# Performance work log

Hardware: AMD Instinct MI355X
Metric: run time of the kernel (lower is better)

The kernel has to match this reference:

```python
import jax, jax.numpy as jnp
import numpy as np

B = 16384      # batch
H = 1024       # latent_dim
C = 2          # output_dim (classes)
PPC = 24       # prototypes per class
P = C * PPC    # 48 total prototypes
EPS = 1e-4


def setup_inputs() -> dict:
    key = jax.random.key(0)
    k1, k2, k3, k4, k5 = jax.random.split(key, 5)
    specific_user = jax.random.normal(k1, (B, H), jnp.float32)
    shared_user = jax.random.normal(k2, (B, H), jnp.float32)
    prototype_vectors = jax.random.normal(k3, (P, H), jnp.float32)
    # last_layer weight set by set_last_layer_incorrect_connection(-0.5):
    # +1 for the prototype's own class, -0.5 elsewhere; shape [C, P]
    cls = np.arange(P) // PPC
    ident = (cls[None, :] == np.arange(C)[:, None]).astype(np.float32)
    last_layer_w = jnp.asarray(ident * 1.0 + (1.0 - ident) * (-0.5))
    # nn.Bilinear(H, H, 1): weight [1, H, H], bias [1]
    bilinear_w = jax.random.normal(k4, (1, H, H), jnp.float32) / np.sqrt(H)
    bilinear_b = jax.random.normal(k5, (1,), jnp.float32) * 0.01
    return {
        "specific_user": specific_user,
        "shared_user": shared_user,
        "prototype_vectors": prototype_vectors,
        "last_layer_w": last_layer_w,
        "bilinear_w": bilinear_w,
        "bilinear_b": bilinear_b,
        "flag": 1,
    }


def reference(specific_user, shared_user, prototype_vectors, last_layer_w,
              bilinear_w, bilinear_b, flag):
    # prototype_distances: squared euclid via mm + norms, then log-similarity
    x2 = jnp.sum(specific_user ** 2, axis=1, keepdims=True)          # [B,1]
    p2 = jnp.sum(prototype_vectors ** 2, axis=1)                     # [P]
    distance = -2.0 * (specific_user @ prototype_vectors.T) + x2 + p2[None, :]  # [B,P]
    similarity = jnp.log((distance + 1.0) / (distance + EPS))        # [B,P]
    logits = similarity @ last_layer_w.T                             # [B,C]

    # select the class's 24 prototypes (flag picks class 1 or 0; static int)
    idx = 1 if flag else 0
    sub = prototype_vectors.reshape(C, PPC, H)[idx]                  # [PPC,H]

    # prototype_subgraph_distances: per original broadcast, each row of
    # all_sim is the batch-mean of the log-similarity -> constant over batch.
    s2 = jnp.sum(sub ** 2, axis=1)                                   # [PPC]
    d = -2.0 * (specific_user @ sub.T) + x2 + s2[None, :]            # [B,PPC]
    sim = jnp.mean(jnp.log((d + 1.0) / (d + EPS)), axis=0)           # [PPC]
    jstar = jnp.argmax(sim)                                          # scalar
    chosen_proto = jnp.broadcast_to(sub[jstar], specific_user.shape) # [B,H]

    # nn.Bilinear(chosen_proto, shared_user) -> [B,1]
    pos = jnp.einsum('bi,ij,bj->b', chosen_proto, bilinear_w[0], shared_user)[:, None] + bilinear_b
    return (pos, shared_user, logits, distance)
```

## Files before the change

kernel.cpp:

```cpp
#include <hip/hip_runtime.h>
#include <hip/hip_bf16.h>

#define BATCH 16384
#define HD    1024
#define NP    48
#define PPC   24
#define EPSV  1e-4f

typedef __attribute__((ext_vector_type(8))) short  short8;
typedef __attribute__((ext_vector_type(4))) float  floatx4;

__device__ __forceinline__ float b2f(unsigned short s) {
    union { unsigned u; float f; } c; c.u = ((unsigned)s) << 16; return c.f;
}
__device__ __forceinline__ unsigned short f2bu(float f) {
    __hip_bfloat16 h = __float2bfloat16(f);
    union { __hip_bfloat16 h; unsigned short u; } c; c.h = h; return c.u;
}

__global__ __launch_bounds__(256) void k_prep(const float* __restrict__ proto,
                                              unsigned short* __restrict__ phi,
                                              unsigned short* __restrict__ plo,
                                              float* __restrict__ p2,
                                              float* __restrict__ vzero,
                                              float* __restrict__ gcol) {
    const int p = blockIdx.x;
    const int tid = threadIdx.x;
    if (p < 4)                        vzero[p * 256 + tid] = 0.f;
    else if (p == 4 && tid < NP)      gcol[tid] = 0.f;

    const float* row = proto + (size_t)p * HD;
    float acc = 0.f;
#pragma unroll
    for (int c = 0; c < 4; ++c) {
        const int k = c * 256 + tid;
        const float f = row[k];
        acc += f * f;
        const unsigned short h = f2bu(f);
        phi[(size_t)p * HD + k] = h;
        plo[(size_t)p * HD + k] = f2bu(f - b2f(h));
    }
#pragma unroll
    for (int m = 32; m >= 1; m >>= 1) acc += __shfl_xor(acc, m, 64);
    __shared__ float wsum[4];
    if ((tid & 63) == 0) wsum[tid >> 6] = acc;
    __syncthreads();
    if (tid == 0) p2[p] = wsum[0] + wsum[1] + wsum[2] + wsum[3];
}

__global__ __launch_bounds__(512, 8) void k_main(
    const float* __restrict__ x,
    const unsigned short* __restrict__ phi,
    const unsigned short* __restrict__ plo,
    const float* __restrict__ llw,
    const float* __restrict__ p2,
    float* __restrict__ gcol,
    float* __restrict__ out_logits,
    float* __restrict__ out_dist)
{
    __shared__ float lacc[8][64][13];
    __shared__ float lx2[8][16];
    const int wave = threadIdx.x >> 6;
    const int lane = threadIdx.x & 63;
    const int quad = lane >> 4;
    const int lr   = lane & 15;
    const int rb   = blockIdx.x * 16;
    const int ko   = wave * 128;

    const float* xr = x + (size_t)(rb + lr) * HD + ko + quad * 8;
    const unsigned short* ph0 = phi + (size_t)lr * HD + ko + quad * 8;
    const unsigned short* ph1 = ph0 + 16 * HD;
    const unsigned short* ph2 = ph0 + 32 * HD;
    const unsigned short* pl0 = plo + (size_t)lr * HD + ko + quad * 8;
    const unsigned short* pl1 = pl0 + 16 * HD;
    const unsigned short* pl2 = pl0 + 32 * HD;

    floatx4 acc0 = {0.f, 0.f, 0.f, 0.f};
    floatx4 acc1 = {0.f, 0.f, 0.f, 0.f};
    floatx4 acc2 = {0.f, 0.f, 0.f, 0.f};
    float x2p = 0.f;

#pragma unroll 2
    for (int kk = 0; kk < 4; ++kk) {
        const floatx4 xa = *(const floatx4*)(xr + kk * 32);
        const floatx4 xb = *(const floatx4*)(xr + kk * 32 + 4);
        short8 ah, al;
#pragma unroll
        for (int j = 0; j < 4; ++j) {
            const float f = xa[j];
            x2p += f * f;
            const unsigned short h = f2bu(f);
            ah[j] = (short)h;
            al[j] = (short)f2bu(f - b2f(h));
        }
#pragma unroll
        for (int j = 0; j < 4; ++j) {
            const float f = xb[j];
            x2p += f * f;
            const unsigned short h = f2bu(f);
            ah[4 + j] = (short)h;
            al[4 + j] = (short)f2bu(f - b2f(h));
        }
        const short8 bh0 = *(const short8*)(ph0 + kk * 32);
        const short8 bh1 = *(const short8*)(ph1 + kk * 32);
        const short8 bh2 = *(const short8*)(ph2 + kk * 32);
        const short8 bl0 = *(const short8*)(pl0 + kk * 32);
        const short8 bl1 = *(const short8*)(pl1 + kk * 32);
        const short8 bl2 = *(const short8*)(pl2 + kk * 32);
        acc0 = __builtin_amdgcn_mfma_f32_16x16x32_bf16(ah, bh0, acc0, 0, 0, 0);
        acc0 = __builtin_amdgcn_mfma_f32_16x16x32_bf16(ah, bl0, acc0, 0, 0, 0);
        acc0 = __builtin_amdgcn_mfma_f32_16x16x32_bf16(al, bh0, acc0, 0, 0, 0);
        acc1 = __builtin_amdgcn_mfma_f32_16x16x32_bf16(ah, bh1, acc1, 0, 0, 0);
        acc1 = __builtin_amdgcn_mfma_f32_16x16x32_bf16(ah, bl1, acc1, 0, 0, 0);
        acc1 = __builtin_amdgcn_mfma_f32_16x16x32_bf16(al, bh1, acc1, 0, 0, 0);
        acc2 = __builtin_amdgcn_mfma_f32_16x16x32_bf16(ah, bh2, acc2, 0, 0, 0);
        acc2 = __builtin_amdgcn_mfma_f32_16x16x32_bf16(ah, bl2, acc2, 0, 0, 0);
        acc2 = __builtin_amdgcn_mfma_f32_16x16x32_bf16(al, bh2, acc2, 0, 0, 0);
    }
    x2p += __shfl_xor(x2p, 16, 64);
    x2p += __shfl_xor(x2p, 32, 64);

#pragma unroll
    for (int r = 0; r < 4; ++r) {
        lacc[wave][lane][r]     = acc0[r];
        lacc[wave][lane][4 + r] = acc1[r];
        lacc[wave][lane][8 + r] = acc2[r];
    }
    if (quad == 0) lx2[wave][lr] = x2p;
    __syncthreads();
    if (wave != 0) return;

    float facc[12];
#pragma unroll
    for (int i = 0; i < 12; ++i) {
        float s = 0.f;
#pragma unroll
        for (int w = 0; w < 8; ++w) s += lacc[w][lane][i];
        facc[i] = s;
    }
    float x2full = 0.f;
#pragma unroll
    for (int w = 0; w < 8; ++w) x2full += lx2[w][lr];

    float s0[4] = {0.f, 0.f, 0.f, 0.f};
    float s1[4] = {0.f, 0.f, 0.f, 0.f};

#pragma unroll
    for (int t = 0; t < 3; ++t) {
        const int p = t * 16 + lr;
        const float p2p = p2[p];
        const float w0 = llw[p];
        const float w1 = llw[NP + p];
        float cst = 0.f;
#pragma unroll
        for (int r = 0; r < 4; ++r) {
            const int row = quad * 4 + r;
            const float x2r = __shfl(x2full, row, 64);
            const float d = -2.f * facc[t * 4 + r] + x2r + p2p;
            out_dist[(size_t)(rb + row) * NP + p] = d;
            const float sim = log1pf((1.f - EPSV) / (d + EPSV));
            s0[r] += sim * w0;
            s1[r] += sim * w1;
            cst += sim;
        }
        cst += __shfl_xor(cst, 16, 64);
        cst += __shfl_xor(cst, 32, 64);
        if (quad == 0) atomicAdd(&gcol[p], cst);
    }

#pragma unroll
    for (int r = 0; r < 4; ++r) {
        float r0 = s0[r], r1 = s1[r];
#pragma unroll
        for (int m = 1; m <= 8; m <<= 1) {
            r0 += __shfl_xor(r0, m, 64);
            r1 += __shfl_xor(r1, m, 64);
        }
        if (lr == 0) {
            const int brow = rb + quad * 4 + r;
            out_logits[(size_t)brow * 2 + 0] = r0;
            out_logits[(size_t)brow * 2 + 1] = r1;
        }
    }
}

__global__ __launch_bounds__(256) void k_matvec(
    const float* __restrict__ proto,
    const float* __restrict__ w2,
    const float* __restrict__ gcol,
    const int* __restrict__ flag,
    float* __restrict__ v)
{
    __shared__ int js;
    const int tid = threadIdx.x;
    const int idx = (flag[0] != 0) ? 1 : 0;
    if (tid == 0) {
        const float* cs = gcol + idx * PPC;
        int bj = 0; float bv = cs[0];
        for (int j = 1; j < PPC; ++j)
            if (cs[j] > bv) { bv = cs[j]; bj = j; }
        js = bj;
    }
    __syncthreads();

    const float* crow = proto + (size_t)(idx * PPC + js) * HD;
    const int i0 = blockIdx.x * 16;
    const int j4 = tid * 4;
    float a0 = 0.f, a1 = 0.f, a2 = 0.f, a3 = 0.f;
#pragma unroll 4
    for (int i = i0; i < i0 + 16; ++i) {
        const float c = crow[i];
        const floatx4 wv = *(const floatx4*)(w2 + (size_t)i * HD + j4);
        a0 += c * wv[0];
        a1 += c * wv[1];
        a2 += c * wv[2];
        a3 += c * wv[3];
    }
    atomicAdd(&v[j4 + 0], a0);
    atomicAdd(&v[j4 + 1], a1);
    atomicAdd(&v[j4 + 2], a2);
    atomicAdd(&v[j4 + 3], a3);
}

__global__ __launch_bounds__(256) void k_pos(
    const float* __restrict__ sh,
    const float* __restrict__ v,
    const float* __restrict__ bias,
    float* __restrict__ out_pos,
    float* __restrict__ out_copy)
{
    const int wave = threadIdx.x >> 6;
    const int lane = threadIdx.x & 63;
    const int b = blockIdx.x * 4 + wave;

    const floatx4* src = (const floatx4*)(sh + (size_t)b * HD);
    floatx4* dst = (floatx4*)(out_copy + (size_t)b * HD);
    const floatx4* vv = (const floatx4*)v;
    float acc = 0.f;
#pragma unroll
    for (int c = 0; c < 4; ++c) {
        const int idx = c * 64 + lane;
        const floatx4 r = src[idx];
        __builtin_nontemporal_store(r, &dst[idx]);
        const floatx4 vr = vv[idx];
#pragma unroll
        for (int j = 0; j < 4; ++j) acc += r[j] * vr[j];
    }
#pragma unroll
    for (int m = 1; m <= 32; m <<= 1) acc += __shfl_xor(acc, m, 64);
    if (lane == 0) out_pos[b] = acc + bias[0];
}

extern "C" void kernel_launch(void* const* d_in, const int* in_sizes, int n_in,
                              void* d_out, int out_size, void* d_ws, size_t ws_size,
                              hipStream_t stream) {
    const float* x     = (const float*)d_in[0];
    const float* sh    = (const float*)d_in[1];
    const float* proto = (const float*)d_in[2];
    const float* llw   = (const float*)d_in[3];
    const float* w2    = (const float*)d_in[4];
    const float* bb    = (const float*)d_in[5];
    const int*   flag  = (const int*)d_in[6];

    float* out = (float*)d_out;
    float* out_pos    = out;
    float* out_copy   = out + BATCH;
    float* out_logits = out + BATCH + BATCH * HD;
    float* out_dist   = out + BATCH + BATCH * HD + BATCH * 2;

    float* ws_v    = (float*)d_ws;
    float* ws_col  = ws_v + 1024;
    float* ws_p2   = ws_v + 1088;
    unsigned short* ws_phi = (unsigned short*)(ws_v + 16384);
    unsigned short* ws_plo = ws_phi + NP * HD;

    k_prep<<<48, 256, 0, stream>>>(proto, ws_phi, ws_plo, ws_p2, ws_v, ws_col);
    k_main<<<1024, 512, 0, stream>>>(x, ws_phi, ws_plo, llw, ws_p2, ws_col, out_logits, out_dist);
    k_matvec<<<64, 256, 0, stream>>>(proto, w2, ws_col, flag, ws_v);
    k_pos<<<4096, 256, 0, stream>>>(sh, ws_v, bb, out_pos, out_copy);
}
```

Before: 256.7 us.

## Split main kernel K-dimension across two blocks with separate finalize kernel

The fused distance/logit kernel is split in two. The first kernel uses 256-thread blocks, each covering half of the K dimension for a 16-row band, and writes partial dot products and row norms to workspace. A new finalize kernel sums the two halves, computes distances, log-similarities, logits and column sums. A fallback single-kernel path with 4 waves each covering 256 of K is used when the workspace is too small. The aim is more, smaller blocks for better occupancy, at the cost of an extra launch and a round trip through global memory for the partials.

After: 258.3 us. Within noise of the previous version (+0.6%).

```diff
diff --git a/kernel.cpp b/kernel.cpp
--- a/kernel.cpp
+++ b/kernel.cpp
@@ -48,24 +48,23 @@
     if (tid == 0) p2[p] = wsum[0] + wsum[1] + wsum[2] + wsum[3];
 }
 
-__global__ __launch_bounds__(512, 8) void k_main(
+__global__ __launch_bounds__(256, 8) void k_mainA(
     const float* __restrict__ x,
     const unsigned short* __restrict__ phi,
     const unsigned short* __restrict__ plo,
-    const float* __restrict__ llw,
-    const float* __restrict__ p2,
-    float* __restrict__ gcol,
-    float* __restrict__ out_logits,
-    float* __restrict__ out_dist)
+    float* __restrict__ dotp,
+    float* __restrict__ x2h)
 {
-    __shared__ float lacc[8][64][13];
-    __shared__ float lx2[8][16];
+    __shared__ float lacc[4][64][13];
+    __shared__ float lx2[4][16];
     const int wave = threadIdx.x >> 6;
     const int lane = threadIdx.x & 63;
     const int quad = lane >> 4;
     const int lr   = lane & 15;
-    const int rb   = blockIdx.x * 16;
-    const int ko   = wave * 128;
+    const int band = blockIdx.x >> 1;
+    const int kh   = blockIdx.x & 1;
+    const int rb   = band * 16;
+    const int ko   = kh * 512 + wave * 128;
 
     const float* xr = x + (size_t)(rb + lr) * HD + ko + quad * 8;
     const unsigned short* ph0 = phi + (size_t)lr * HD + ko + quad * 8;
@@ -132,15 +131,158 @@
 
     float facc[12];
 #pragma unroll
-    for (int i = 0; i < 12; ++i) {
-        float s = 0.f;
-#pragma unroll
-        for (int w = 0; w < 8; ++w) s += lacc[w][lane][i];
-        facc[i] = s;
-    }
-    float x2full = 0.f;
-#pragma unroll
-    for (int w = 0; w < 8; ++w) x2full += lx2[w][lr];
+    for (int i = 0; i < 12; ++i)
+        facc[i] = lacc[0][lane][i] + lacc[1][lane][i] + lacc[2][lane][i] + lacc[3][lane][i];
+    const float x2full = lx2[0][lr] + lx2[1][lr] + lx2[2][lr] + lx2[3][lr];
+
+    float* drow = dotp + ((size_t)kh * 1024 + band) * (16 * NP);
+#pragma unroll
+    for (int t = 0; t < 3; ++t)
+#pragma unroll
+        for (int r = 0; r < 4; ++r)
+            drow[(quad * 4 + r) * NP + t * 16 + lr] = facc[t * 4 + r];
+    if (quad == 0) x2h[((size_t)kh * 1024 + band) * 16 + lr] = x2full;
+}
+
+__global__ __launch_bounds__(256) void k_fin(
+    const float* __restrict__ dotp,
+    const float* __restrict__ x2h,
+    const float* __restrict__ p2,
+    const float* __restrict__ llw,
+    float* __restrict__ gcol,
+    float* __restrict__ out_logits,
+    float* __restrict__ out_dist)
+{
+    __shared__ float gsum[NP];
+    const int wave = threadIdx.x >> 6;
+    const int lane = threadIdx.x & 63;
+    const int band = blockIdx.x;
+    if (threadIdx.x < NP) gsum[threadIdx.x] = 0.f;
+    __syncthreads();
+
+    const float p2p = (lane < NP) ? p2[lane] : 0.f;
+    const float w0  = (lane < NP) ? llw[lane] : 0.f;
+    const float w1  = (lane < NP) ? llw[NP + lane] : 0.f;
+    const float* dA = dotp + (size_t)band * (16 * NP);
+    const float* dB = dotp + ((size_t)1024 + band) * (16 * NP);
+    float csum = 0.f;
+
+#pragma unroll
+    for (int r = 0; r < 4; ++r) {
+        const int rrow = wave * 4 + r;
+        const int row  = band * 16 + rrow;
+        const float x2 = x2h[band * 16 + rrow] + x2h[1024 * 16 + band * 16 + rrow];
+        float sim = 0.f;
+        if (lane < NP) {
+            const float dot = dA[rrow * NP + lane] + dB[rrow * NP + lane];
+            const float d = -2.f * dot + x2 + p2p;
+            out_dist[(size_t)row * NP + lane] = d;
+            sim = log1pf((1.f - EPSV) / (d + EPSV));
+        }
+        csum += sim;
+        float r0 = sim * w0, r1 = sim * w1;
+#pragma unroll
+        for (int m = 1; m <= 32; m <<= 1) {
+            r0 += __shfl_xor(r0, m, 64);
+            r1 += __shfl_xor(r1, m, 64);
+        }
+        if (lane == 0) {
+            out_logits[(size_t)row * 2 + 0] = r0;
+            out_logits[(size_t)row * 2 + 1] = r1;
+        }
+    }
+    if (lane < NP) atomicAdd(&gsum[lane], csum);
+    __syncthreads();
+    if (threadIdx.x < NP) atomicAdd(&gcol[threadIdx.x], gsum[threadIdx.x]);
+}
+
+__global__ __launch_bounds__(256, 4) void k_main_fb(
+    const float* __restrict__ x,
+    const unsigned short* __restrict__ phi,
+    const unsigned short* __restrict__ plo,
+    const float* __restrict__ llw,
+    const float* __restrict__ p2,
+    float* __restrict__ gcol,
+    float* __restrict__ out_logits,
+    float* __restrict__ out_dist)
+{
+    __shared__ float lacc[4][64][13];
+    __shared__ float lx2[4][16];
+    const int wave = threadIdx.x >> 6;
+    const int lane = threadIdx.x & 63;
+    const int quad = lane >> 4;
+    const int lr   = lane & 15;
+    const int rb   = blockIdx.x * 16;
+    const int ko   = wave * 256;
+
+    const float* xr = x + (size_t)(rb + lr) * HD + ko + quad * 8;
+    const unsigned short* ph0 = phi + (size_t)lr * HD + ko + quad * 8;
+    const unsigned short* ph1 = ph0 + 16 * HD;
+    const unsigned short* ph2 = ph0 + 32 * HD;
+    const unsigned short* pl0 = plo + (size_t)lr * HD + ko + quad * 8;
+    const unsigned short* pl1 = pl0 + 16 * HD;
+    const unsigned short* pl2 = pl0 + 32 * HD;
+
+    floatx4 acc0 = {0.f, 0.f, 0.f, 0.f};
+    floatx4 acc1 = {0.f, 0.f, 0.f, 0.f};
+    floatx4 acc2 = {0.f, 0.f, 0.f, 0.f};
+    float x2p = 0.f;
+
+#pragma unroll 2
+    for (int kk = 0; kk < 8; ++kk) {
+        const floatx4 xa = *(const floatx4*)(xr + kk * 32);
+        const floatx4 xb = *(const floatx4*)(xr + kk * 32 + 4);
+        short8 ah, al;
+#pragma unroll
+        for (int j = 0; j < 4; ++j) {
+            const float f = xa[j];
+            x2p += f * f;
+            const unsigned short h = f2bu(f);
+            ah[j] = (short)h;
+            al[j] = (short)f2bu(f - b2f(h));
+        }
+#pragma unroll
+        for (int j = 0; j < 4; ++j) {
+            const float f = xb[j];
+            x2p += f * f;
+            const unsigned short h = f2bu(f);
+            ah[4 + j] = (short)h;
+            al[4 + j] = (short)f2bu(f - b2f(h));
+        }
+        const short8 bh0 = *(const short8*)(ph0 + kk * 32);
+        const short8 bh1 = *(const short8*)(ph1 + kk * 32);
+        const short8 bh2 = *(const short8*)(ph2 + kk * 32);
+        const short8 bl0 = *(const short8*)(pl0 + kk * 32);
+        const short8 bl1 = *(const short8*)(pl1 + kk * 32);
+        const short8 bl2 = *(const short8*)(pl2 + kk * 32);
+        acc0 = __builtin_amdgcn_mfma_f32_16x16x32_bf16(ah, bh0, acc0, 0, 0, 0);
+        acc0 = __builtin_amdgcn_mfma_f32_16x16x32_bf16(ah, bl0, acc0, 0, 0, 0);
+        acc0 = __builtin_amdgcn_mfma_f32_16x16x32_bf16(al, bh0, acc0, 0, 0, 0);
+        acc1 = __builtin_amdgcn_mfma_f32_16x16x32_bf16(ah, bh1, acc1, 0, 0, 0);
+        acc1 = __builtin_amdgcn_mfma_f32_16x16x32_bf16(ah, bl1, acc1, 0, 0, 0);
+        acc1 = __builtin_amdgcn_mfma_f32_16x16x32_bf16(al, bh1, acc1, 0, 0, 0);
+        acc2 = __builtin_amdgcn_mfma_f32_16x16x32_bf16(ah, bh2, acc2, 0, 0, 0);
+        acc2 = __builtin_amdgcn_mfma_f32_16x16x32_bf16(ah, bl2, acc2, 0, 0, 0);
+        acc2 = __builtin_amdgcn_mfma_f32_16x16x32_bf16(al, bh2, acc2, 0, 0, 0);
+    }
+    x2p += __shfl_xor(x2p, 16, 64);
+    x2p += __shfl_xor(x2p, 32, 64);
+
+#pragma unroll
+    for (int r = 0; r < 4; ++r) {
+        lacc[wave][lane][r]     = acc0[r];
+        lacc[wave][lane][4 + r] = acc1[r];
+        lacc[wave][lane][8 + r] = acc2[r];
+    }
+    if (quad == 0) lx2[wave][lr] = x2p;
+    __syncthreads();
+    if (wave != 0) return;
+
+    float facc[12];
+#pragma unroll
+    for (int i = 0; i < 12; ++i)
+        facc[i] = lacc[0][lane][i] + lacc[1][lane][i] + lacc[2][lane][i] + lacc[3][lane][i];
+    const float x2full = lx2[0][lr] + lx2[1][lr] + lx2[2][lr] + lx2[3][lr];
 
     float s0[4] = {0.f, 0.f, 0.f, 0.f};
     float s1[4] = {0.f, 0.f, 0.f, 0.f};
@@ -273,9 +415,17 @@
     float* ws_p2   = ws_v + 1088;
     unsigned short* ws_phi = (unsigned short*)(ws_v + 16384);
     unsigned short* ws_plo = ws_phi + NP * HD;
+    float* ws_dot  = ws_v + 65536;
+    float* ws_x2   = ws_v + 1638400;
+    const bool big_ws = ws_size >= (size_t)1671168 * 4;
 
     k_prep<<<48, 256, 0, stream>>>(proto, ws_phi, ws_plo, ws_p2, ws_v, ws_col);
-    k_main<<<1024, 512, 0, stream>>>(x, ws_phi, ws_plo, llw, ws_p2, ws_col, out_logits, out_dist);
+    if (big_ws) {
+        k_mainA<<<2048, 256, 0, stream>>>(x, ws_phi, ws_plo, ws_dot, ws_x2);
+        k_fin<<<1024, 256, 0, stream>>>(ws_dot, ws_x2, ws_p2, llw, ws_col, out_logits, out_dist);
+    } else {
+        k_main_fb<<<1024, 256, 0, stream>>>(x, ws_phi, ws_plo, llw, ws_p2, ws_col, out_logits, out_dist);
+    }
     k_matvec<<<64, 256, 0, stream>>>(proto, w2, ws_col, flag, ws_v);
     k_pos<<<4096, 256, 0, stream>>>(sh, ws_v, bb, out_pos, out_copy);
 }
```
